# Kernel tuning notes

Measured on AMD Instinct MI355X. Metric: run time of the kernel, lower is better.

Reference implementation:

```python
import jax, jax.numpy as jnp
import numpy as np

T, K, E, H, I = 2048, 8, 32, 1024, 768


def setup_inputs() -> dict:
    key = jax.random.key(0)
    k0, k1, k2, k3, k4, k5 = jax.random.split(key, 6)
    sh = 1.0 / np.sqrt(H).astype(np.float32)
    si = 1.0 / np.sqrt(I).astype(np.float32)
    return {
        "hidden_states": jax.random.normal(k0, (T, H), jnp.float32),
        "top_k_index": jax.random.randint(k1, (T, K), 0, E),
        "top_k_weights": jax.random.uniform(k2, (T, K), jnp.float32),
        "gate_proj": jax.random.normal(k3, (E, I, H), jnp.float32) * sh,
        "up_proj": jax.random.normal(k4, (E, I, H), jnp.float32) * sh,
        "down_proj": jax.random.normal(k5, (E, H, I), jnp.float32) * si,
    }


def reference(hidden_states, top_k_index, top_k_weights, gate_proj, up_proj, down_proj):
    # Tokens not routed to expert e get combine weight 0, so summing the
    # weighted per-expert outputs over all experts reproduces the original
    # gather -> SwiGLU MLP -> scale -> index_add_ exactly (duplicated expert
    # hits within a token's top-k sum, matching repeated index_add_).
    n_tok = hidden_states.shape[0]
    n_exp = gate_proj.shape[0]
    combine = jnp.zeros((n_tok, n_exp), hidden_states.dtype)
    combine = combine.at[jnp.arange(n_tok)[:, None], top_k_index].add(top_k_weights)

    def body(acc, xs):
        g_w, u_w, d_w, w_e = xs  # g_w,u_w: [I,H]; d_w: [H,I]; w_e: [T]
        h = jax.nn.silu(hidden_states @ g_w.T) * (hidden_states @ u_w.T)  # [T,I]
        y = h @ d_w.T  # [T,H]
        return acc + y * w_e[:, None], None

    out, _ = jax.lax.scan(
        body,
        jnp.zeros_like(hidden_states),
        (gate_proj, up_proj, down_proj, combine.T),
    )
    return out
```

## Files before the change

### kernel.cpp

```cpp
#include <hip/hip_runtime.h>

#define T_TOK 2048
#define TOPK  8
#define NEXP  32
#define HDIM  1024
#define IDIM  768
#define NPAIR (T_TOK * TOPK)
#define BM 128
#define BK 32
#define MT_MAX (NPAIR / BM + NEXP)

typedef __attribute__((ext_vector_type(8))) short short8;
typedef __attribute__((ext_vector_type(4))) float f32x4;

__device__ __forceinline__ unsigned short f2bf(float f) {
    unsigned x = __float_as_uint(f);
    unsigned r = x + 0x7fffu + ((x >> 16) & 1u);
    return (unsigned short)(r >> 16);
}
__device__ __forceinline__ float bf2f(unsigned short u) {
    return __uint_as_float(((unsigned)u) << 16);
}

__device__ __forceinline__ void gl_lds16(const unsigned short* g, void* l) {
    __builtin_amdgcn_global_load_lds((const __attribute__((address_space(1))) void*)g,
                                     (__attribute__((address_space(3))) void*)l, 16, 0, 0);
}

__global__ void k_conv(const float* __restrict__ src, unsigned short* __restrict__ dst, int n4) {
    int i = blockIdx.x * 256 + threadIdx.x;
    if (i < n4) {
        float4 v = ((const float4*)src)[i];
        ushort4 o;
        o.x = f2bf(v.x); o.y = f2bf(v.y); o.z = f2bf(v.z); o.w = f2bf(v.w);
        ((ushort4*)dst)[i] = o;
    }
}

__global__ void k_init(int* counts) {
    if (threadIdx.x < NEXP) counts[threadIdx.x] = 0;
}

__global__ void k_hist(const int* __restrict__ idx, int* __restrict__ counts) {
    int p = blockIdx.x * 256 + threadIdx.x;
    atomicAdd(&counts[idx[p]], 1);
}

__global__ void k_scan(const int* __restrict__ counts, int* __restrict__ offsets,
                       int* __restrict__ mtb, int* __restrict__ cursor) {
    if (threadIdx.x == 0) {
        int tot = 0, mt = 0;
        for (int e = 0; e < NEXP; ++e) {
            offsets[e] = tot; mtb[e] = mt;
            tot += counts[e];
            mt += (counts[e] + BM - 1) / BM;
        }
        offsets[NEXP] = tot; mtb[NEXP] = mt;
    }
    if (threadIdx.x < NEXP) cursor[threadIdx.x] = 0;
}

__global__ void k_scatter(const int* __restrict__ idx, int* __restrict__ cursor,
                          const int* __restrict__ offsets, int* __restrict__ pair_token,
                          int* __restrict__ pair_slot) {
    int p = blockIdx.x * 256 + threadIdx.x;
    int e = idx[p];
    int pos = atomicAdd(&cursor[e], 1);
    int slot = offsets[e] + pos;
    pair_token[slot] = p >> 3;
    pair_slot[p] = slot;
}

__global__ __launch_bounds__(256) void k_gateup(
    const unsigned short* __restrict__ hid_bf, const unsigned short* __restrict__ gate_bf,
    const unsigned short* __restrict__ up_bf, const int* __restrict__ pair_token,
    const int* __restrict__ offsets, const int* __restrict__ mtb,
    unsigned short* __restrict__ h_mid)
{
    __shared__ short8 sA[512], sBg[256], sBu[256];
    __shared__ int sInfo[4];
    int tid = threadIdx.x;
    if (tid == 0) {
        int mt = blockIdx.x;
        if (mt >= mtb[NEXP]) { sInfo[0] = -1; }
        else {
            int e = 0;
            while (mtb[e + 1] <= mt) e++;
            sInfo[0] = e; sInfo[1] = offsets[e];
            sInfo[2] = offsets[e + 1] - offsets[e];
            sInfo[3] = (mt - mtb[e]) * BM;
        }
    }
    __syncthreads();
    int e = sInfo[0];
    if (e < 0) return;
    int off = sInfo[1], Me = sInfo[2], mrow0 = sInfo[3];
    int n0 = blockIdx.y * 64;

    int wave = tid >> 6, lane = tid & 63, quad = lane >> 4, l16 = lane & 15;

    int m0 = wave * 32 + l16, m1 = m0 + 16;
    int rp0 = mrow0 + m0, rp1 = mrow0 + m1;
    int tok0 = (rp0 < Me) ? pair_token[off + rp0] : 0;
    int tok1 = (rp1 < Me) ? pair_token[off + rp1] : 0;
    const unsigned short* aG0 = hid_bf + (size_t)tok0 * HDIM + quad * 8;
    const unsigned short* aG1 = hid_bf + (size_t)tok1 * HDIM + quad * 8;
    int nB = n0 + wave * 16 + l16;
    const unsigned short* gG = gate_bf + ((size_t)e * IDIM + nB) * HDIM + quad * 8;
    const unsigned short* uG = up_bf   + ((size_t)e * IDIM + nB) * HDIM + quad * 8;
    void* ldsA0 = (void*)&sA[wave * 128];
    void* ldsA1 = (void*)&sA[wave * 128 + 64];
    void* ldsBg = (void*)&sBg[wave * 64];
    void* ldsBu = (void*)&sBu[wave * 64];

    int wm = (wave & 1) * 64, wn = (wave >> 1) * 32;
    int aBase = (wm >> 4) * 64 + quad * 16 + l16;
    int bBase = (wn >> 4) * 64 + quad * 16 + l16;

    f32x4 zero = {0.f, 0.f, 0.f, 0.f};
    f32x4 accg[4][2], accu[4][2];
#pragma unroll
    for (int i = 0; i < 4; ++i)
#pragma unroll
        for (int j = 0; j < 2; ++j) { accg[i][j] = zero; accu[i][j] = zero; }

    for (int k0 = 0; k0 < HDIM; k0 += BK) {
        gl_lds16(aG0 + k0, ldsA0);
        gl_lds16(aG1 + k0, ldsA1);
        gl_lds16(gG + k0, ldsBg);
        gl_lds16(uG + k0, ldsBu);
        __syncthreads();
        short8 af[4];
#pragma unroll
        for (int fm = 0; fm < 4; ++fm) af[fm] = sA[aBase + fm * 64];
#pragma unroll
        for (int fn = 0; fn < 2; ++fn) {
            short8 bg = sBg[bBase + fn * 64];
            short8 bu = sBu[bBase + fn * 64];
#pragma unroll
            for (int fm = 0; fm < 4; ++fm) {
                accg[fm][fn] = __builtin_amdgcn_mfma_f32_16x16x32_bf16(af[fm], bg, accg[fm][fn], 0, 0, 0);
                accu[fm][fn] = __builtin_amdgcn_mfma_f32_16x16x32_bf16(af[fm], bu, accu[fm][fn], 0, 0, 0);
            }
        }
        __syncthreads();
    }

#pragma unroll
    for (int fm = 0; fm < 4; ++fm)
#pragma unroll
        for (int fn = 0; fn < 2; ++fn)
#pragma unroll
            for (int r = 0; r < 4; ++r) {
                int mloc = wm + fm * 16 + quad * 4 + r;
                int prow = mrow0 + mloc;
                if (prow < Me) {
                    int col = n0 + wn + fn * 16 + l16;
                    float g = accg[fm][fn][r], u = accu[fm][fn][r];
                    float h = g / (1.f + __expf(-g)) * u;
                    h_mid[(size_t)(off + prow) * IDIM + col] = f2bf(h);
                }
            }
}

__global__ __launch_bounds__(256) void k_down(
    const unsigned short* __restrict__ h_mid, const unsigned short* __restrict__ down_bf,
    const int* __restrict__ offsets, const int* __restrict__ mtb,
    unsigned short* __restrict__ y_pair)
{
    __shared__ short8 sA[512], sB[512];
    __shared__ int sInfo[4];
    int tid = threadIdx.x;
    if (tid == 0) {
        int mt = blockIdx.x;
        if (mt >= mtb[NEXP]) { sInfo[0] = -1; }
        else {
            int e = 0;
            while (mtb[e + 1] <= mt) e++;
            sInfo[0] = e; sInfo[1] = offsets[e];
            sInfo[2] = offsets[e + 1] - offsets[e];
            sInfo[3] = (mt - mtb[e]) * BM;
        }
    }
    __syncthreads();
    int e = sInfo[0];
    if (e < 0) return;
    int off = sInfo[1], Me = sInfo[2], mrow0 = sInfo[3];
    int n0 = blockIdx.y * 128;

    int wave = tid >> 6, lane = tid & 63, quad = lane >> 4, l16 = lane & 15;

    int m0 = wave * 32 + l16, m1 = m0 + 16;
    int rp0 = mrow0 + m0; if (rp0 >= Me) rp0 = 0;
    int rp1 = mrow0 + m1; if (rp1 >= Me) rp1 = 0;
    const unsigned short* aG0 = h_mid + (size_t)(off + rp0) * IDIM + quad * 8;
    const unsigned short* aG1 = h_mid + (size_t)(off + rp1) * IDIM + quad * 8;
    int nb0 = n0 + wave * 32 + l16, nb1 = nb0 + 16;
    const unsigned short* bG0 = down_bf + ((size_t)e * HDIM + nb0) * IDIM + quad * 8;
    const unsigned short* bG1 = down_bf + ((size_t)e * HDIM + nb1) * IDIM + quad * 8;
    void* ldsA0 = (void*)&sA[wave * 128];
    void* ldsA1 = (void*)&sA[wave * 128 + 64];
    void* ldsB0 = (void*)&sB[wave * 128];
    void* ldsB1 = (void*)&sB[wave * 128 + 64];

    int wm = (wave & 1) * 64, wn = (wave >> 1) * 64;
    int aBase = (wm >> 4) * 64 + quad * 16 + l16;
    int bBase = (wn >> 4) * 64 + quad * 16 + l16;

    f32x4 zero = {0.f, 0.f, 0.f, 0.f};
    f32x4 acc[4][4];
#pragma unroll
    for (int i = 0; i < 4; ++i)
#pragma unroll
        for (int j = 0; j < 4; ++j) acc[i][j] = zero;

    for (int k0 = 0; k0 < IDIM; k0 += BK) {
        gl_lds16(aG0 + k0, ldsA0);
        gl_lds16(aG1 + k0, ldsA1);
        gl_lds16(bG0 + k0, ldsB0);
        gl_lds16(bG1 + k0, ldsB1);
        __syncthreads();
        short8 af[4];
#pragma unroll
        for (int fm = 0; fm < 4; ++fm) af[fm] = sA[aBase + fm * 64];
#pragma unroll
        for (int fn = 0; fn < 4; ++fn) {
            short8 bf = sB[bBase + fn * 64];
#pragma unroll
            for (int fm = 0; fm < 4; ++fm)
                acc[fm][fn] = __builtin_amdgcn_mfma_f32_16x16x32_bf16(af[fm], bf, acc[fm][fn], 0, 0, 0);
        }
        __syncthreads();
    }

#pragma unroll
    for (int fm = 0; fm < 4; ++fm)
#pragma unroll
        for (int fn = 0; fn < 4; ++fn)
#pragma unroll
            for (int r = 0; r < 4; ++r) {
                int mloc = wm + fm * 16 + quad * 4 + r;
                int prow = mrow0 + mloc;
                if (prow < Me) {
                    int col = n0 + wn + fn * 16 + l16;
                    y_pair[(size_t)(off + prow) * HDIM + col] = f2bf(acc[fm][fn][r]);
                }
            }
}

__global__ void k_reduce(const unsigned short* __restrict__ y_pair,
                         const int* __restrict__ pair_slot,
                         const float* __restrict__ topw, float* __restrict__ out)
{
    int t = blockIdx.x;
    __shared__ int ss[TOPK];
    __shared__ float sw[TOPK];
    if (threadIdx.x < TOPK) {
        ss[threadIdx.x] = pair_slot[t * TOPK + threadIdx.x];
        sw[threadIdx.x] = topw[t * TOPK + threadIdx.x];
    }
    __syncthreads();
    int c = threadIdx.x * 4;
    float a0 = 0.f, a1 = 0.f, a2 = 0.f, a3 = 0.f;
    for (int k = 0; k < TOPK; ++k) {
        const unsigned short* yr = y_pair + (size_t)ss[k] * HDIM + c;
        uint2 v = *(const uint2*)yr;
        float w = sw[k];
        a0 += w * bf2f((unsigned short)(v.x & 0xffff));
        a1 += w * bf2f((unsigned short)(v.x >> 16));
        a2 += w * bf2f((unsigned short)(v.y & 0xffff));
        a3 += w * bf2f((unsigned short)(v.y >> 16));
    }
    float4 o = {a0, a1, a2, a3};
    *(float4*)(out + (size_t)t * HDIM + c) = o;
}

extern "C" void kernel_launch(void* const* d_in, const int* in_sizes, int n_in,
                              void* d_out, int out_size, void* d_ws, size_t ws_size,
                              hipStream_t stream) {
    (void)in_sizes; (void)n_in; (void)out_size; (void)ws_size;
    const float* hidden = (const float*)d_in[0];
    const int*   tki    = (const int*)d_in[1];
    const float* tkw    = (const float*)d_in[2];
    const float* gate   = (const float*)d_in[3];
    const float* up     = (const float*)d_in[4];
    const float* down   = (const float*)d_in[5];
    float* out = (float*)d_out;

    char* w = (char*)d_ws;
    unsigned short* h_mid   = (unsigned short*)w;
    unsigned short* hid_bf  = (unsigned short*)(w + 25165824);
    unsigned short* gate_bf = (unsigned short*)(w + 29360128);
    unsigned short* up_bf   = (unsigned short*)(w + 79691776);
    unsigned short* down_bf = gate_bf;
    unsigned short* y_pair  = up_bf;
    int* ib = (int*)(w + 130023424);
    int* pair_token = ib;
    int* pair_slot  = ib + NPAIR;
    int* counts     = ib + 2 * NPAIR;
    int* cursor     = counts + NEXP;
    int* offsets    = cursor + NEXP;
    int* mtb        = offsets + NEXP + 1;

    const int W4 = NEXP * IDIM * HDIM / 4;
    const int H4 = T_TOK * HDIM / 4;

    k_init<<<1, 64, 0, stream>>>(counts);
    k_hist<<<NPAIR / 256, 256, 0, stream>>>(tki, counts);
    k_scan<<<1, 64, 0, stream>>>(counts, offsets, mtb, cursor);
    k_scatter<<<NPAIR / 256, 256, 0, stream>>>(tki, cursor, offsets, pair_token, pair_slot);

    k_conv<<<(H4 + 255) / 256, 256, 0, stream>>>(hidden, hid_bf, H4);
    k_conv<<<(W4 + 255) / 256, 256, 0, stream>>>(gate, gate_bf, W4);
    k_conv<<<(W4 + 255) / 256, 256, 0, stream>>>(up, up_bf, W4);

    k_gateup<<<dim3(MT_MAX, IDIM / 64), 256, 0, stream>>>(hid_bf, gate_bf, up_bf,
                                                          pair_token, offsets, mtb, h_mid);

    k_conv<<<(W4 + 255) / 256, 256, 0, stream>>>(down, down_bf, W4);

    k_down<<<dim3(MT_MAX, HDIM / 128), 256, 0, stream>>>(h_mid, down_bf, offsets, mtb, y_pair);
    k_reduce<<<T_TOK, 256, 0, stream>>>(y_pair, pair_slot, tkw, out);
}
```

Baseline: 581.0 us.

## Widen N tiles in gate/up and down GEMMs and fuse weight conversions

Doubles the N tile of the gate/up GEMM (64→128) and the down GEMM (128→256), with more per-wave loads and accumulators. Each gathered activation tile is now reused across more output columns, which cuts redundant A loads and block count. It also adds __launch_bounds__(256,2) and merges the gate and up fp32→bf16 conversions into one launch. The costs are higher register and LDS pressure and fewer blocks to fill the GPU. The merged conversion relies on up_bf sitting directly after gate_bf in the workspace.

```diff
diff --git a/kernel.cpp b/kernel.cpp
--- a/kernel.cpp
+++ b/kernel.cpp
@@ -27,6 +27,19 @@
                                      (__attribute__((address_space(3))) void*)l, 16, 0, 0);
 }
 
+__global__ void k_conv2(const float* __restrict__ src0, const float* __restrict__ src1,
+                        unsigned short* __restrict__ dst, int n4each) {
+    int i = blockIdx.x * 256 + threadIdx.x;
+    const float* s = (i < n4each) ? src0 : src1;
+    int j = (i < n4each) ? i : i - n4each;
+    if (i < 2 * n4each) {
+        float4 v = ((const float4*)s)[j];
+        ushort4 o;
+        o.x = f2bf(v.x); o.y = f2bf(v.y); o.z = f2bf(v.z); o.w = f2bf(v.w);
+        ((ushort4*)dst)[i] = o;
+    }
+}
+
 __global__ void k_conv(const float* __restrict__ src, unsigned short* __restrict__ dst, int n4) {
     int i = blockIdx.x * 256 + threadIdx.x;
     if (i < n4) {
@@ -71,13 +84,13 @@
     pair_slot[p] = slot;
 }
 
-__global__ __launch_bounds__(256) void k_gateup(
+__global__ __launch_bounds__(256, 2) void k_gateup(
     const unsigned short* __restrict__ hid_bf, const unsigned short* __restrict__ gate_bf,
     const unsigned short* __restrict__ up_bf, const int* __restrict__ pair_token,
     const int* __restrict__ offsets, const int* __restrict__ mtb,
     unsigned short* __restrict__ h_mid)
 {
-    __shared__ short8 sA[512], sBg[256], sBu[256];
+    __shared__ short8 sA[512], sBg[512], sBu[512];
     __shared__ int sInfo[4];
     int tid = threadIdx.x;
     if (tid == 0) {
@@ -95,7 +108,7 @@
     int e = sInfo[0];
     if (e < 0) return;
     int off = sInfo[1], Me = sInfo[2], mrow0 = sInfo[3];
-    int n0 = blockIdx.y * 64;
+    int n0 = blockIdx.y * 128;
 
     int wave = tid >> 6, lane = tid & 63, quad = lane >> 4, l16 = lane & 15;
 
@@ -105,36 +118,35 @@
     int tok1 = (rp1 < Me) ? pair_token[off + rp1] : 0;
     const unsigned short* aG0 = hid_bf + (size_t)tok0 * HDIM + quad * 8;
     const unsigned short* aG1 = hid_bf + (size_t)tok1 * HDIM + quad * 8;
-    int nB = n0 + wave * 16 + l16;
-    const unsigned short* gG = gate_bf + ((size_t)e * IDIM + nB) * HDIM + quad * 8;
-    const unsigned short* uG = up_bf   + ((size_t)e * IDIM + nB) * HDIM + quad * 8;
-    void* ldsA0 = (void*)&sA[wave * 128];
-    void* ldsA1 = (void*)&sA[wave * 128 + 64];
-    void* ldsBg = (void*)&sBg[wave * 64];
-    void* ldsBu = (void*)&sBu[wave * 64];
-
-    int wm = (wave & 1) * 64, wn = (wave >> 1) * 32;
+    const unsigned short* gG0 = gate_bf + ((size_t)e * IDIM + n0 + m0) * HDIM + quad * 8;
+    const unsigned short* gG1 = gate_bf + ((size_t)e * IDIM + n0 + m1) * HDIM + quad * 8;
+    const unsigned short* uG0 = up_bf + ((size_t)e * IDIM + n0 + m0) * HDIM + quad * 8;
+    const unsigned short* uG1 = up_bf + ((size_t)e * IDIM + n0 + m1) * HDIM + quad * 8;
+    void* ldsA0 = (void*)&sA[wave * 128];  void* ldsA1 = (void*)&sA[wave * 128 + 64];
+    void* ldsG0 = (void*)&sBg[wave * 128]; void* ldsG1 = (void*)&sBg[wave * 128 + 64];
+    void* ldsU0 = (void*)&sBu[wave * 128]; void* ldsU1 = (void*)&sBu[wave * 128 + 64];
+
+    int wm = (wave & 1) * 64, wn = (wave >> 1) * 64;
     int aBase = (wm >> 4) * 64 + quad * 16 + l16;
     int bBase = (wn >> 4) * 64 + quad * 16 + l16;
 
     f32x4 zero = {0.f, 0.f, 0.f, 0.f};
-    f32x4 accg[4][2], accu[4][2];
+    f32x4 accg[4][4], accu[4][4];
 #pragma unroll
     for (int i = 0; i < 4; ++i)
 #pragma unroll
-        for (int j = 0; j < 2; ++j) { accg[i][j] = zero; accu[i][j] = zero; }
+        for (int j = 0; j < 4; ++j) { accg[i][j] = zero; accu[i][j] = zero; }
 
     for (int k0 = 0; k0 < HDIM; k0 += BK) {
-        gl_lds16(aG0 + k0, ldsA0);
-        gl_lds16(aG1 + k0, ldsA1);
-        gl_lds16(gG + k0, ldsBg);
-        gl_lds16(uG + k0, ldsBu);
+        gl_lds16(aG0 + k0, ldsA0); gl_lds16(aG1 + k0, ldsA1);
+        gl_lds16(gG0 + k0, ldsG0); gl_lds16(gG1 + k0, ldsG1);
+        gl_lds16(uG0 + k0, ldsU0); gl_lds16(uG1 + k0, ldsU1);
         __syncthreads();
         short8 af[4];
 #pragma unroll
         for (int fm = 0; fm < 4; ++fm) af[fm] = sA[aBase + fm * 64];
 #pragma unroll
-        for (int fn = 0; fn < 2; ++fn) {
+        for (int fn = 0; fn < 4; ++fn) {
             short8 bg = sBg[bBase + fn * 64];
             short8 bu = sBu[bBase + fn * 64];
 #pragma unroll
@@ -149,7 +161,7 @@
 #pragma unroll
     for (int fm = 0; fm < 4; ++fm)
 #pragma unroll
-        for (int fn = 0; fn < 2; ++fn)
+        for (int fn = 0; fn < 4; ++fn)
 #pragma unroll
             for (int r = 0; r < 4; ++r) {
                 int mloc = wm + fm * 16 + quad * 4 + r;
@@ -163,12 +175,12 @@
             }
 }
 
-__global__ __launch_bounds__(256) void k_down(
+__global__ __launch_bounds__(256, 2) void k_down(
     const unsigned short* __restrict__ h_mid, const unsigned short* __restrict__ down_bf,
     const int* __restrict__ offsets, const int* __restrict__ mtb,
     unsigned short* __restrict__ y_pair)
 {
-    __shared__ short8 sA[512], sB[512];
+    __shared__ short8 sA[512], sB[1024];
     __shared__ int sInfo[4];
     int tid = threadIdx.x;
     if (tid == 0) {
@@ -186,7 +198,7 @@
     int e = sInfo[0];
     if (e < 0) return;
     int off = sInfo[1], Me = sInfo[2], mrow0 = sInfo[3];
-    int n0 = blockIdx.y * 128;
+    int n0 = blockIdx.y * 256;
 
     int wave = tid >> 6, lane = tid & 63, quad = lane >> 4, l16 = lane & 15;
 
@@ -195,36 +207,35 @@
     int rp1 = mrow0 + m1; if (rp1 >= Me) rp1 = 0;
     const unsigned short* aG0 = h_mid + (size_t)(off + rp0) * IDIM + quad * 8;
     const unsigned short* aG1 = h_mid + (size_t)(off + rp1) * IDIM + quad * 8;
-    int nb0 = n0 + wave * 32 + l16, nb1 = nb0 + 16;
-    const unsigned short* bG0 = down_bf + ((size_t)e * HDIM + nb0) * IDIM + quad * 8;
-    const unsigned short* bG1 = down_bf + ((size_t)e * HDIM + nb1) * IDIM + quad * 8;
-    void* ldsA0 = (void*)&sA[wave * 128];
-    void* ldsA1 = (void*)&sA[wave * 128 + 64];
-    void* ldsB0 = (void*)&sB[wave * 128];
-    void* ldsB1 = (void*)&sB[wave * 128 + 64];
-
-    int wm = (wave & 1) * 64, wn = (wave >> 1) * 64;
+    const unsigned short* bG0 = down_bf + ((size_t)e * HDIM + n0 + wave * 64 + l16) * IDIM + quad * 8;
+    const unsigned short* bG1 = bG0 + (size_t)16 * IDIM;
+    const unsigned short* bG2 = bG0 + (size_t)32 * IDIM;
+    const unsigned short* bG3 = bG0 + (size_t)48 * IDIM;
+    void* ldsA0 = (void*)&sA[wave * 128];      void* ldsA1 = (void*)&sA[wave * 128 + 64];
+    void* ldsB0 = (void*)&sB[wave * 256];      void* ldsB1 = (void*)&sB[wave * 256 + 64];
+    void* ldsB2 = (void*)&sB[wave * 256 + 128]; void* ldsB3 = (void*)&sB[wave * 256 + 192];
+
+    int wm = (wave & 1) * 64, wn = (wave >> 1) * 128;
     int aBase = (wm >> 4) * 64 + quad * 16 + l16;
     int bBase = (wn >> 4) * 64 + quad * 16 + l16;
 
     f32x4 zero = {0.f, 0.f, 0.f, 0.f};
-    f32x4 acc[4][4];
+    f32x4 acc[4][8];
 #pragma unroll
     for (int i = 0; i < 4; ++i)
 #pragma unroll
-        for (int j = 0; j < 4; ++j) acc[i][j] = zero;
+        for (int j = 0; j < 8; ++j) acc[i][j] = zero;
 
     for (int k0 = 0; k0 < IDIM; k0 += BK) {
-        gl_lds16(aG0 + k0, ldsA0);
-        gl_lds16(aG1 + k0, ldsA1);
-        gl_lds16(bG0 + k0, ldsB0);
-        gl_lds16(bG1 + k0, ldsB1);
+        gl_lds16(aG0 + k0, ldsA0); gl_lds16(aG1 + k0, ldsA1);
+        gl_lds16(bG0 + k0, ldsB0); gl_lds16(bG1 + k0, ldsB1);
+        gl_lds16(bG2 + k0, ldsB2); gl_lds16(bG3 + k0, ldsB3);
         __syncthreads();
         short8 af[4];
 #pragma unroll
         for (int fm = 0; fm < 4; ++fm) af[fm] = sA[aBase + fm * 64];
 #pragma unroll
-        for (int fn = 0; fn < 4; ++fn) {
+        for (int fn = 0; fn < 8; ++fn) {
             short8 bf = sB[bBase + fn * 64];
 #pragma unroll
             for (int fm = 0; fm < 4; ++fm)
@@ -236,7 +247,7 @@
 #pragma unroll
     for (int fm = 0; fm < 4; ++fm)
 #pragma unroll
-        for (int fn = 0; fn < 4; ++fn)
+        for (int fn = 0; fn < 8; ++fn)
 #pragma unroll
             for (int r = 0; r < 4; ++r) {
                 int mloc = wm + fm * 16 + quad * 4 + r;
@@ -311,14 +322,13 @@
     k_scatter<<<NPAIR / 256, 256, 0, stream>>>(tki, cursor, offsets, pair_token, pair_slot);
 
     k_conv<<<(H4 + 255) / 256, 256, 0, stream>>>(hidden, hid_bf, H4);
-    k_conv<<<(W4 + 255) / 256, 256, 0, stream>>>(gate, gate_bf, W4);
-    k_conv<<<(W4 + 255) / 256, 256, 0, stream>>>(up, up_bf, W4);
-
-    k_gateup<<<dim3(MT_MAX, IDIM / 64), 256, 0, stream>>>(hid_bf, gate_bf, up_bf,
-                                                          pair_token, offsets, mtb, h_mid);
+    k_conv2<<<(2 * W4 + 255) / 256, 256, 0, stream>>>(gate, up, gate_bf, W4);
+
+    k_gateup<<<dim3(MT_MAX, IDIM / 128), 256, 0, stream>>>(hid_bf, gate_bf, up_bf,
+                                                           pair_token, offsets, mtb, h_mid);
 
     k_conv<<<(W4 + 255) / 256, 256, 0, stream>>>(down, down_bf, W4);
 
-    k_down<<<dim3(MT_MAX, HDIM / 128), 256, 0, stream>>>(h_mid, down_bf, offsets, mtb, y_pair);
+    k_down<<<dim3(MT_MAX, HDIM / 256), 256, 0, stream>>>(h_mid, down_bf, offsets, mtb, y_pair);
     k_reduce<<<T_TOK, 256, 0, stream>>>(y_pair, pair_slot, tkw, out);
 }
```

New measurement: 558.8 us. 3.8% less time.
